# Kernel optimization log

Measured on AMD Instinct MI355X. Metric: run time of the kernel, lower is better.

Reference implementation:

```python
import jax, jax.numpy as jnp
import numpy as np

N = 50000      # nodes
E = 800000     # edges (avg degree 16)
F_IN = 128
H = 128        # hidden_channels
C = 10         # num_classes
S = 5          # Chebyshev order K
B = 8          # graphs in batch


def setup_inputs() -> dict:
    key = jax.random.key(0)
    ks = jax.random.split(key, 9)
    x = jax.random.normal(ks[0], (N, F_IN), jnp.float32)
    edge_index = jax.random.randint(ks[1], (2, E), 0, N, dtype=jnp.int64)
    batch = jnp.sort(jax.random.randint(ks[2], (N,), 0, B, dtype=jnp.int64))
    lambda_max = 2.0 * jnp.ones((B,), jnp.float32)
    W1 = jax.random.normal(ks[3], (S, F_IN, H), jnp.float32) * 0.05
    b1 = jax.random.normal(ks[4], (H,), jnp.float32) * 0.05
    W2 = jax.random.normal(ks[5], (S, H, H), jnp.float32) * 0.05
    b2 = jax.random.normal(ks[6], (H,), jnp.float32) * 0.05
    Wlin = jax.random.normal(ks[7], (H, C), jnp.float32) * 0.05
    blin = jax.random.normal(ks[8], (C,), jnp.float32) * 0.05
    return {"x": x, "edge_index": edge_index, "batch": batch,
            "lambda_max": lambda_max, "W1": W1, "b1": b1,
            "W2": W2, "b2": b2, "Wlin": Wlin, "blin": blin}


def _cheb_conv(x, row, col, w_edge, diag, W, b):
    # scaled Laplacian matvec: L_hat v = scatter(w_edge * v[col] -> row) + diag * v
    def Lhat(v):
        msg = v[col] * w_edge[:, None]                       # [E, d]
        return jax.ops.segment_sum(msg, row, num_segments=N) + diag[:, None] * v

    Tx0 = x
    out = Tx0 @ W[0]
    Tx1 = Lhat(Tx0)
    out = out + Tx1 @ W[1]
    for k in range(2, W.shape[0]):                           # Chebyshev recurrence
        Tx2 = 2.0 * Lhat(Tx1) - Tx0
        out = out + Tx2 @ W[k]
        Tx0, Tx1 = Tx1, Tx2
    return out + b


def reference(x, edge_index, batch, lambda_max, W1, b1, W2, b2, Wlin, blin):
    row, col = edge_index[0], edge_index[1]
    # sym-normalized Laplacian L = I - D^{-1/2} A D^{-1/2}; L_hat = 2L/lambda_max - I
    deg = jax.ops.segment_sum(jnp.ones((E,), x.dtype), row, num_segments=N)
    dis = jnp.where(deg > 0, jax.lax.rsqrt(jnp.maximum(deg, 1e-12)), 0.0)
    lam_e = lambda_max[batch[row]]                           # per-edge lambda_max
    w_edge = -2.0 * dis[row] * dis[col] / lam_e              # off-diagonal of L_hat
    diag = 2.0 / lambda_max[batch] - 1.0                     # diagonal of L_hat per node

    h = jax.nn.relu(_cheb_conv(x, row, col, w_edge, diag, W1, b1))
    h = jax.nn.relu(_cheb_conv(h, row, col, w_edge, diag, W2, b2))

    # global_mean_pool over batch assignment
    sums = jax.ops.segment_sum(h, batch, num_segments=B)     # [B, H]
    counts = jax.ops.segment_sum(jnp.ones((N, 1), h.dtype), batch, num_segments=B)
    pooled = sums / jnp.maximum(counts, 1.0)
    return pooled @ Wlin + blin                              # [B, C] logits (softmax unused in forward)
```

## Files before the change

### kernel.cpp

```cpp
#include <hip/hip_runtime.h>
#include <stdint.h>

typedef __attribute__((ext_vector_type(8))) short bf16x8;
typedef __attribute__((ext_vector_type(4))) float f32x4;

__device__ __forceinline__ float bf16lo_to_f(uint32_t u) { return __uint_as_float(u << 16); }
__device__ __forceinline__ float bf16hi_to_f(uint32_t u) { return __uint_as_float(u & 0xffff0000u); }
__device__ __forceinline__ uint16_t f_to_bf16(float f) {
    uint32_t u = __float_as_uint(f);
    uint32_t r = u + 0x7fff + ((u >> 16) & 1);
    return (uint16_t)(r >> 16);
}


#define BINCH 4096

__global__ void __launch_bounds__(256) k_pre1(
        const int* __restrict__ row, int* __restrict__ bhist,
        const float* __restrict__ W1, uint16_t* __restrict__ Wt1,
        const float* __restrict__ W2, uint16_t* __restrict__ Wt2,
        const float* __restrict__ x, uint16_t* __restrict__ Txb,
        int E, int N) {
    __shared__ int sh[256];
    int t = threadIdx.x, b = blockIdx.x;
    int gstride = gridDim.x * 256;
    sh[t] = 0;
    __syncthreads();
    for (int e = b * 256 + t; e < E; e += gstride)
        atomicAdd(&sh[row[e] >> 8], 1);
    __syncthreads();
    if (sh[t]) atomicAdd(&bhist[t], sh[t]);
    for (int i = b * 256 + t; i < 2 * 128 * 640; i += gstride) {
        int ii = i;
        const float* W = W1; uint16_t* Wt = Wt1;
        if (ii >= 128 * 640) { ii -= 128 * 640; W = W2; Wt = Wt2; }
        int o = ii / 640, kk = ii % 640;
        Wt[(size_t)o * 640 + kk] = f_to_bf16(W[(size_t)kk * 128 + o]);
    }
    {
        int lane = t & 63;
        int gw = b * 4 + (t >> 6);
        int tw = gridDim.x * 4;
        for (int n = gw; n < N; n += tw) {
            float2 v = ((const float2*)x)[(size_t)n * 64 + lane];
            uint32_t p = (uint32_t)f_to_bf16(v.x) | ((uint32_t)f_to_bf16(v.y) << 16);
            ((uint32_t*)Txb)[(size_t)n * 64 + lane] = p;
        }
    }
    if (b == 0) {
        int lane = t & 63;
        size_t ss32 = (size_t)(N + 1) * 64;
        for (int s = t >> 6; s < 5; s += 4)
            ((uint32_t*)Txb)[(size_t)s * ss32 + (size_t)N * 64 + lane] = 0u;
    }
}

__global__ void k_bscan(const int* __restrict__ bhist, int* __restrict__ gbase,
                        int* __restrict__ gcur, int nbk) {
    __shared__ int sh[256];
    int t = threadIdx.x;
    int v = t < nbk ? bhist[t] : 0;
    sh[t] = v;
    __syncthreads();
    for (int o = 1; o < 256; o <<= 1) {
        int u = (t >= o) ? sh[t - o] : 0;
        __syncthreads();
        sh[t] += u;
        __syncthreads();
    }
    gbase[t] = sh[t] - v;
    gcur[t] = sh[t] - v;
    if (t == 255) gbase[256] = sh[255];
}

__global__ void __launch_bounds__(256) k_bin(const int* __restrict__ row,
        const int* __restrict__ col, int* __restrict__ gcur,
        uint32_t* __restrict__ bout, int E) {
    __shared__ uint32_t stage[BINCH];
    __shared__ int hist[256], hscan[256], hcur[256], gofs[256];
    int t = threadIdx.x;
    int e0 = blockIdx.x * BINCH;
    int ecnt = min(BINCH, E - e0);
    hist[t] = 0;
    __syncthreads();
    for (int i = t; i < ecnt; i += 256)
        atomicAdd(&hist[row[e0 + i] >> 8], 1);
    __syncthreads();
    int v = hist[t];
    hscan[t] = v;
    __syncthreads();
    for (int o = 1; o < 256; o <<= 1) {
        int u = (t >= o) ? hscan[t - o] : 0;
        __syncthreads();
        hscan[t] += u;
        __syncthreads();
    }
    hcur[t] = hscan[t] - v;
    __syncthreads();
    for (int i = t; i < ecnt; i += 256) {
        int r = row[e0 + i];
        int p = atomicAdd(&hcur[r >> 8], 1);
        stage[p] = (uint32_t)(r & 255) | ((uint32_t)col[e0 + i] << 8);
    }
    __syncthreads();
    if (v > 0) gofs[t] = atomicAdd(&gcur[t], v);
    __syncthreads();
    for (int i = t; i < ecnt; i += 256) {
        int lo = 0, hi = 255;
        while (lo < hi) { int mid = (lo + hi) >> 1; if (hscan[mid] > i) hi = mid; else lo = mid + 1; }
        int b = lo;
        int local = i - (hscan[b] - hist[b]);
        bout[gofs[b] + local] = stage[i];
    }
}

__global__ void __launch_bounds__(256) k_deg2(const uint32_t* __restrict__ bout,
        const int* __restrict__ gbase, int* __restrict__ deg,
        int* __restrict__ psum, int N) {
    __shared__ int cnt[256];
    __shared__ int red[256];
    int t = threadIdx.x, b = blockIdx.x;
    cnt[t] = 0;
    __syncthreads();
    int s = gbase[b], epos = gbase[b + 1];
    for (int i = s + t; i < epos; i += 256)
        atomicAdd(&cnt[bout[i] & 255], 1);
    __syncthreads();
    int n = b * 256 + t;
    int d = cnt[t];
    if (n < N) deg[n] = d;
    red[t] = (n < N) ? ((d + 7) & ~7) : 0;
    __syncthreads();
    for (int o = 128; o > 0; o >>= 1) {
        if (t < o) red[t] += red[t + o];
        __syncthreads();
    }
    if (t == 0) psum[b] = red[0];
}

__global__ void k_offs(const int* __restrict__ deg, const int* __restrict__ psum,
                       int* __restrict__ offs,
                       const int* __restrict__ batch, const float* __restrict__ lam,
                       float* __restrict__ dis, float* __restrict__ diag,
                       uint4* __restrict__ nh,
                       int N, int nb) {
    __shared__ int pre[256];
    __shared__ int sh[256];
    int t = threadIdx.x, b = blockIdx.x;
    pre[t] = (t < b) ? psum[t] : 0;
    __syncthreads();
    for (int o = 128; o > 0; o >>= 1) {
        if (t < o) pre[t] += pre[t + o];
        __syncthreads();
    }
    int base = pre[0];
    __syncthreads();
    int idx = b * 256 + t;
    int d = idx < N ? deg[idx] : 0;
    int v = (d + 7) & ~7;
    sh[t] = v;
    __syncthreads();
    for (int o = 1; o < 256; o <<= 1) {
        int u = (t >= o) ? sh[t - o] : 0;
        __syncthreads();
        sh[t] += u;
        __syncthreads();
    }
    if (idx < N) {
        int beg = base + sh[t] - v;
        float dgv = 2.f / lam[batch[idx]] - 1.f;
        offs[idx] = beg;
        dis[idx] = d > 0 ? rsqrtf((float)d) : 0.f;
        diag[idx] = dgv;
        nh[idx] = make_uint4((uint32_t)beg, (uint32_t)(base + sh[t]),
                             __float_as_uint(dgv), 0u);
    }
    if (b == nb - 1 && t == 255) offs[N] = base + sh[255];
}

__global__ void __launch_bounds__(256) k_ew(const uint32_t* __restrict__ bout,
        const int* __restrict__ gbase, const int* __restrict__ offs,
        const float* __restrict__ dis, const float* __restrict__ diag,
        uint32_t* __restrict__ ew, int N) {
    __shared__ int cur[256];
    __shared__ int bs0[256];
    __shared__ float srw[256];
    int t = threadIdx.x, b = blockIdx.x;
    int n = b * 256 + t;
    int o0 = n < N ? offs[n] : 0;
    cur[t] = 0;
    bs0[t] = o0;
    srw[t] = (n < N) ? (-dis[n] * (diag[n] + 1.0f)) : 0.f;
    __syncthreads();
    int s = gbase[b], epos = gbase[b + 1];
    for (int i = s + t; i < epos; i += 256) {
        uint32_t v = bout[i];
        int r = (int)(v & 255u);
        int c = (int)(v >> 8);
        int idx = atomicAdd(&cur[r], 1);
        float w = srw[r] * dis[c];
        int pos = bs0[r] + (idx & ~7) + ((idx & 1) << 2) + ((idx >> 1) & 3);
        ew[pos] = (uint32_t)c | ((uint32_t)f_to_bf16(w) << 16);
    }
    __syncthreads();
    if (n < N) {
        int cnt = cur[t];
        int pe = (cnt + 7) & ~7;
        for (int i = cnt; i < pe; i++) {
            int pos = o0 + (i & ~7) + ((i & 1) << 2) + ((i >> 1) & 3);
            ew[pos] = (uint32_t)N;
        }
    }
}

__global__ void __launch_bounds__(256) k_lhat(uint16_t* __restrict__ Txb,
        const uint4* __restrict__ nh, const uint32_t* __restrict__ ew,
        int N,
        int src, int dst, int prev, float alpha, int use_prev) {
    int n = (blockIdx.x * blockDim.x + threadIdx.x) >> 6;
    int lane = threadIdx.x & 63;
    if (n >= N) return;
    int h = lane >> 5, g = lane & 31;
    size_t sb = (size_t)(N + 1) * 256;
    const uint8_t* srcs = (const uint8_t*)Txb + (size_t)src * sb;
    uint32_t g8 = (uint32_t)g * 8;
    uint4 hh = nh[n];
    int e = (int)hh.x, end = (int)hh.y;
    float dgn = __uint_as_float(hh.z);
    float a0 = 0.f, a1 = 0.f, a2 = 0.f, a3 = 0.f;
    int npk = (end - e) >> 3;
    const uint4* ep = (const uint4*)(ew + e + h * 4);
    int pk = 0;
    while (pk < npk) {
        if (npk - pk >= 2) {
            uint4 c0 = ep[pk * 2];
            uint4 c1 = ep[pk * 2 + 2];
            uint2 q[8]; float w[8];
#pragma unroll
            for (int u = 0; u < 4; u++) {
                uint32_t cw = (&c0.x)[u];
                w[u] = __uint_as_float(cw & 0xffff0000u);
                q[u] = *(const uint2*)(srcs + ((cw & 0xffffu) << 8) + g8);
            }
#pragma unroll
            for (int u = 0; u < 4; u++) {
                uint32_t cw = (&c1.x)[u];
                w[4 + u] = __uint_as_float(cw & 0xffff0000u);
                q[4 + u] = *(const uint2*)(srcs + ((cw & 0xffffu) << 8) + g8);
            }
#pragma unroll
            for (int u = 0; u < 8; u++) {
                a0 = fmaf(w[u], bf16lo_to_f(q[u].x), a0);
                a1 = fmaf(w[u], bf16hi_to_f(q[u].x), a1);
                a2 = fmaf(w[u], bf16lo_to_f(q[u].y), a2);
                a3 = fmaf(w[u], bf16hi_to_f(q[u].y), a3);
            }
            pk += 2;
        } else {
            uint4 c0 = ep[pk * 2];
#pragma unroll
            for (int u = 0; u < 4; u++) {
                uint32_t cw = (&c0.x)[u];
                float w = __uint_as_float(cw & 0xffff0000u);
                uint2 q = *(const uint2*)(srcs + ((cw & 0xffffu) << 8) + g8);
                a0 = fmaf(w, bf16lo_to_f(q.x), a0);
                a1 = fmaf(w, bf16hi_to_f(q.x), a1);
                a2 = fmaf(w, bf16lo_to_f(q.y), a2);
                a3 = fmaf(w, bf16hi_to_f(q.y), a3);
            }
            pk += 1;
        }
    }
    a0 += __shfl_xor(a0, 32);
    a1 += __shfl_xor(a1, 32);
    a2 += __shfl_xor(a2, 32);
    a3 += __shfl_xor(a3, 32);
    if (h == 0) {
        size_t ro = (size_t)n * 256 + g8;
        uint2 qs = *(const uint2*)(srcs + ro);
        a0 = fmaf(dgn, bf16lo_to_f(qs.x), a0);
        a1 = fmaf(dgn, bf16hi_to_f(qs.x), a1);
        a2 = fmaf(dgn, bf16lo_to_f(qs.y), a2);
        a3 = fmaf(dgn, bf16hi_to_f(qs.y), a3);
        float f0 = alpha * a0, f1 = alpha * a1, f2 = alpha * a2, f3 = alpha * a3;
        if (use_prev) {
            uint2 qp = *(const uint2*)((const uint8_t*)Txb + (size_t)prev * sb + ro);
            f0 -= bf16lo_to_f(qp.x);
            f1 -= bf16hi_to_f(qp.x);
            f2 -= bf16lo_to_f(qp.y);
            f3 -= bf16hi_to_f(qp.y);
        }
        uint2 pk2;
        pk2.x = (uint32_t)f_to_bf16(f0) | ((uint32_t)f_to_bf16(f1) << 16);
        pk2.y = (uint32_t)f_to_bf16(f2) | ((uint32_t)f_to_bf16(f3) << 16);
        *(uint2*)((uint8_t*)Txb + (size_t)dst * sb + ro) = pk2;
    }
}

#define BM 128
#define BK 64
#define LDT 72
#define LDC 132

__global__ void __launch_bounds__(256) k_gemm(
        const uint16_t* __restrict__ A, size_t sstride,
        const uint16_t* __restrict__ Bt,
        const float* __restrict__ bias,
        uint16_t* __restrict__ out2b,
        float* __restrict__ pooled,
        const int* __restrict__ batch,
        int M, int Kdim) {
    __shared__ uint16_t smem[BM * LDT + 128 * LDT];
    uint16_t* As = smem;
    uint16_t* Bs = smem + BM * LDT;
    uint16_t* Ct = smem;
    int t = threadIdx.x;
    int w = t >> 6, lane = t & 63;
    int row0 = blockIdx.x * BM;
    int mrow = (w >> 1) * 64, ncol = (w & 1) * 64;

    int ar[4], akc[4];
#pragma unroll
    for (int rep = 0; rep < 4; rep++) {
        int d = rep * 256 + t;
        ar[rep] = d >> 3; akc[rep] = d & 7;
    }

    f32x4 acc[4][4];
#pragma unroll
    for (int i = 0; i < 4; i++)
#pragma unroll
        for (int j = 0; j < 4; j++) acc[i][j] = (f32x4){0.f, 0.f, 0.f, 0.f};

    bf16x8 pa[4], pb[4];
#pragma unroll
    for (int rep = 0; rep < 4; rep++) {
        int grow = row0 + ar[rep];
        int kk = akc[rep] * 8;
        bf16x8 va = {0, 0, 0, 0, 0, 0, 0, 0};
        if (grow < M)
            va = *(const bf16x8*)(A + (size_t)(kk >> 7) * sstride + (size_t)grow * 128 + (kk & 127));
        pa[rep] = va;
        pb[rep] = *(const bf16x8*)(Bt + (size_t)ar[rep] * Kdim + kk);
    }

    for (int k0 = 0; k0 < Kdim; k0 += BK) {
#pragma unroll
        for (int rep = 0; rep < 4; rep++) {
            *(bf16x8*)(&As[ar[rep] * LDT + akc[rep] * 8]) = pa[rep];
            *(bf16x8*)(&Bs[ar[rep] * LDT + akc[rep] * 8]) = pb[rep];
        }
        __syncthreads();
        int kn = k0 + BK;
        if (kn < Kdim) {
#pragma unroll
            for (int rep = 0; rep < 4; rep++) {
                int grow = row0 + ar[rep];
                int kk = kn + akc[rep] * 8;
                bf16x8 va = {0, 0, 0, 0, 0, 0, 0, 0};
                if (grow < M)
                    va = *(const bf16x8*)(A + (size_t)(kk >> 7) * sstride + (size_t)grow * 128 + (kk & 127));
                pa[rep] = va;
                pb[rep] = *(const bf16x8*)(Bt + (size_t)ar[rep] * Kdim + kk);
            }
        }
#pragma unroll
        for (int ks = 0; ks < BK; ks += 32) {
            bf16x8 af[4], bfr[4];
#pragma unroll
            for (int i = 0; i < 4; i++) {
                int r = mrow + i * 16 + (lane & 15);
                af[i] = *(const bf16x8*)(&As[r * LDT + ks + (lane >> 4) * 8]);
            }
#pragma unroll
            for (int j = 0; j < 4; j++) {
                int c = ncol + j * 16 + (lane & 15);
                bfr[j] = *(const bf16x8*)(&Bs[c * LDT + ks + (lane >> 4) * 8]);
            }
#pragma unroll
            for (int i = 0; i < 4; i++)
#pragma unroll
                for (int j = 0; j < 4; j++)
                    acc[i][j] = __builtin_amdgcn_mfma_f32_16x16x32_bf16(af[i], bfr[j], acc[i][j], 0, 0, 0);
        }
        __syncthreads();
    }

#pragma unroll
    for (int j = 0; j < 4; j++) {
        int c = ncol + j * 16 + (lane & 15);
        float bv = bias[c];
#pragma unroll
        for (int i = 0; i < 4; i++) {
            int rloc = mrow + i * 16 + (lane >> 4) * 4;
#pragma unroll
            for (int r = 0; r < 4; r++) {
                float v = acc[i][j][r] + bv;
                v = v > 0.f ? v : 0.f;
                Ct[(rloc + r) * LDC + c] = f_to_bf16(v);
            }
        }
    }
    __syncthreads();

    if (out2b) {
#pragma unroll
        for (int rep = 0; rep < 8; rep++) {
            int d = rep * 256 + t;
            int r = d >> 4, c8 = (d & 15) * 8;
            int grow = row0 + r;
            if (grow < M) {
                bf16x8 v = *(const bf16x8*)(&Ct[r * LDC + c8]);
                *(bf16x8*)(out2b + (size_t)grow * 128 + c8) = v;
            }
        }
    }
    if (pooled) {
        int f = t & 127, r0 = (t >> 7) * 64;
        float accp = 0.f;
        int curb = -1;
        for (int r = r0; r < r0 + 64; ++r) {
            int grow = row0 + r;
            if (grow >= M) break;
            int b = batch[grow];
            if (b != curb) {
                if (curb >= 0) atomicAdd(&pooled[curb * 128 + f], accp);
                accp = 0.f; curb = b;
            }
            accp += __uint_as_float(((uint32_t)Ct[r * LDC + f]) << 16);
        }
        if (curb >= 0) atomicAdd(&pooled[curb * 128 + f], accp);
    }
}

__global__ void k_final(const float* __restrict__ pooled, const int* __restrict__ batch,
                        const float* __restrict__ Wlin, const float* __restrict__ blin,
                        float* __restrict__ out, int N, int B_, int C_) {
    __shared__ int cnt[64];
    int t = threadIdx.x;
    if (t < B_) {
        auto lb = [&](int v) {
            int lo = 0, hi = N;
            while (lo < hi) {
                int mid = (lo + hi) >> 1;
                if (batch[mid] < v) lo = mid + 1; else hi = mid;
            }
            return lo;
        };
        cnt[t] = lb(t + 1) - lb(t);
    }
    __syncthreads();
    if (t < B_ * C_) {
        int b = t / C_, c = t % C_;
        float inv = 1.f / fmaxf((float)cnt[b], 1.f);
        float acc = blin[c];
        for (int f = 0; f < 128; ++f) acc += pooled[b * 128 + f] * inv * Wlin[f * C_ + c];
        out[t] = acc;
    }
}

extern "C" void kernel_launch(void* const* d_in, const int* in_sizes, int n_in,
                              void* d_out, int out_size, void* d_ws, size_t ws_size,
                              hipStream_t stream) {
    const float* x    = (const float*)d_in[0];
    const int*   edge = (const int*)d_in[1];
    const int*   batch= (const int*)d_in[2];
    const float* lam  = (const float*)d_in[3];
    const float* W1   = (const float*)d_in[4];
    const float* b1   = (const float*)d_in[5];
    const float* W2   = (const float*)d_in[6];
    const float* b2   = (const float*)d_in[7];
    const float* Wlin = (const float*)d_in[8];
    const float* blin = (const float*)d_in[9];
    const int E  = in_sizes[1] / 2;
    const int N  = in_sizes[2];
    const int B_ = in_sizes[3];
    const int* row = edge;
    const int* col = edge + E;

    char* ws = (char*)d_ws;
    size_t off = 0;
    auto take = [&](size_t bytes) -> char* {
        char* p = ws + off;
        off = (off + bytes + 255) & ~(size_t)255;
        return p;
    };
    uint16_t* Txb    = (uint16_t*)take((size_t)5 * (N + 1) * 128 * 2);
    uint32_t* ew     = (uint32_t*)take(((size_t)E + 8 * (size_t)N) * 4);
    int*      deg    = (int*)take((size_t)N * 4);
    int*      offs   = (int*)take((size_t)(N + 1) * 4);
    float*    dis    = (float*)take((size_t)N * 4);
    float*    diag   = (float*)take((size_t)N * 4);
    uint4*    nh     = (uint4*)take((size_t)N * 16);
    uint16_t* Wt1    = (uint16_t*)take((size_t)128 * 640 * 2);
    uint16_t* Wt2    = (uint16_t*)take((size_t)128 * 640 * 2);
    float*    pooled = (float*)take((size_t)B_ * 128 * 4);
    int*      bhist  = (int*)take(257 * 4);
    int*      gbase  = (int*)take(257 * 4);
    int*      gcur   = (int*)take(257 * 4);
    const int nb = (N + 255) / 256;
    int*      psum   = (int*)take((size_t)nb * 4);
    uint32_t* bout   = (uint32_t*)((char*)Txb + (size_t)4 * (N + 1) * 256);

    hipMemsetAsync(pooled, 0, (size_t)B_ * 128 * 4 + 257 * 4, stream);

    const int nchunks = (E + BINCH - 1) / BINCH;

    k_pre1<<<1024, 256, 0, stream>>>(row, bhist, W1, Wt1, W2, Wt2, x, Txb, E, N);
    k_bscan<<<1, 256, 0, stream>>>(bhist, gbase, gcur, nb);
    k_bin<<<nchunks, 256, 0, stream>>>(row, col, gcur, bout, E);
    k_deg2<<<nb, 256, 0, stream>>>(bout, gbase, deg, psum, N);
    k_offs<<<nb, 256, 0, stream>>>(deg, psum, offs, batch, lam, dis, diag, nh, N, nb);
    k_ew<<<nb, 256, 0, stream>>>(bout, gbase, offs, dis, diag, ew, N);

    const int lblocks = (N + 3) / 4;
    const int gblocks = (N + BM - 1) / BM;
    const size_t ss = (size_t)(N + 1) * 128;

    k_lhat<<<lblocks, 256, 0, stream>>>(Txb, nh, ew, N, 0, 1, 0, 1.f, 0);
    k_lhat<<<lblocks, 256, 0, stream>>>(Txb, nh, ew, N, 1, 2, 0, 2.f, 1);
    k_lhat<<<lblocks, 256, 0, stream>>>(Txb, nh, ew, N, 2, 3, 1, 2.f, 1);
    k_lhat<<<lblocks, 256, 0, stream>>>(Txb, nh, ew, N, 3, 4, 2, 2.f, 1);
    k_gemm<<<gblocks, 256, 0, stream>>>(Txb, ss, Wt1, b1,
                                        Txb , (float*)nullptr, batch, N, 640);

    k_lhat<<<lblocks, 256, 0, stream>>>(Txb, nh, ew, N, 0, 1, 0, 1.f, 0);
    k_lhat<<<lblocks, 256, 0, stream>>>(Txb, nh, ew, N, 1, 2, 0, 2.f, 1);
    k_lhat<<<lblocks, 256, 0, stream>>>(Txb, nh, ew, N, 2, 3, 1, 2.f, 1);
    k_lhat<<<lblocks, 256, 0, stream>>>(Txb, nh, ew, N, 3, 4, 2, 2.f, 1);
    k_gemm<<<gblocks, 256, 0, stream>>>(Txb, ss, Wt2, b2,
                                        (uint16_t*)nullptr, pooled, batch, N, 640);

    k_final<<<1, 128, 0, stream>>>(pooled, batch, Wlin, blin, (float*)d_out, N, B_, 10);
}
```

Before: 468.5 us.

## Load GEMM tiles straight into LDS via global_load_lds with XOR swizzle

The GEMM kernel's A and B tile staging now uses the global-to-LDS direct load builtin instead of loading into registers and then storing to LDS. The padded LDS layout becomes an unpadded 64-wide layout with an XOR swizzle on the k offset to avoid bank conflicts. This is meant to cut VGPR use and the LDS-store instructions. In exchange it drops the register prefetch that overlapped the next tile's global loads with MFMA work, and it drops the row-bounds check on A, so the last row block reads past M.

```diff
diff --git a/kernel.cpp b/kernel.cpp
--- a/kernel.cpp
+++ b/kernel.cpp
@@ -1,5 +1,9 @@
 #include <hip/hip_runtime.h>
 #include <stdint.h>
+
+#ifndef __has_builtin
+#define __has_builtin(x) 0
+#endif
 
 typedef __attribute__((ext_vector_type(8))) short bf16x8;
 typedef __attribute__((ext_vector_type(4))) float f32x4;
@@ -10,6 +14,15 @@
     uint32_t u = __float_as_uint(f);
     uint32_t r = u + 0x7fff + ((u >> 16) & 1);
     return (uint16_t)(r >> 16);
+}
+
+__device__ __forceinline__ void dma16(const uint16_t* g, uint16_t* lds, int lane) {
+#if __has_builtin(__builtin_amdgcn_global_load_lds)
+    __builtin_amdgcn_global_load_lds((const __attribute__((address_space(1))) void*)g,
+                                     (__attribute__((address_space(3))) void*)lds, 16, 0, 0);
+#else
+    *(bf16x8*)(lds + lane * 8) = *(const bf16x8*)g;
+#endif
 }
 
 
@@ -298,8 +311,7 @@
 }
 
 #define BM 128
-#define BK 64
-#define LDT 72
+#define BKS 64
 #define LDC 132
 
 __global__ void __launch_bounds__(256) k_gemm(
@@ -310,20 +322,22 @@
         float* __restrict__ pooled,
         const int* __restrict__ batch,
         int M, int Kdim) {
-    __shared__ uint16_t smem[BM * LDT + 128 * LDT];
+    __shared__ uint16_t smem[128 * LDC];
     uint16_t* As = smem;
-    uint16_t* Bs = smem + BM * LDT;
+    uint16_t* Bs = smem + 128 * 64;
     uint16_t* Ct = smem;
     int t = threadIdx.x;
     int w = t >> 6, lane = t & 63;
     int row0 = blockIdx.x * BM;
     int mrow = (w >> 1) * 64, ncol = (w & 1) * 64;
 
-    int ar[4], akc[4];
+    int ar[4], swz[4];
 #pragma unroll
     for (int rep = 0; rep < 4; rep++) {
         int d = rep * 256 + t;
-        ar[rep] = d >> 3; akc[rep] = d & 7;
+        int a = d >> 3, kc = d & 7;
+        ar[rep] = a;
+        swz[rep] = (kc * 8) ^ ((a & 7) << 3);
     }
 
     f32x4 acc[4][4];
@@ -332,50 +346,35 @@
 #pragma unroll
         for (int j = 0; j < 4; j++) acc[i][j] = (f32x4){0.f, 0.f, 0.f, 0.f};
 
-    bf16x8 pa[4], pb[4];
-#pragma unroll
-    for (int rep = 0; rep < 4; rep++) {
-        int grow = row0 + ar[rep];
-        int kk = akc[rep] * 8;
-        bf16x8 va = {0, 0, 0, 0, 0, 0, 0, 0};
-        if (grow < M)
-            va = *(const bf16x8*)(A + (size_t)(kk >> 7) * sstride + (size_t)grow * 128 + (kk & 127));
-        pa[rep] = va;
-        pb[rep] = *(const bf16x8*)(Bt + (size_t)ar[rep] * Kdim + kk);
-    }
-
-    for (int k0 = 0; k0 < Kdim; k0 += BK) {
+    for (int k0 = 0; k0 < Kdim; k0 += BKS) {
+        int slotbase = (k0 >> 7) * (int)0;
+        (void)slotbase;
 #pragma unroll
         for (int rep = 0; rep < 4; rep++) {
-            *(bf16x8*)(&As[ar[rep] * LDT + akc[rep] * 8]) = pa[rep];
-            *(bf16x8*)(&Bs[ar[rep] * LDT + akc[rep] * 8]) = pb[rep];
-        }
-        __syncthreads();
-        int kn = k0 + BK;
-        if (kn < Kdim) {
-#pragma unroll
-            for (int rep = 0; rep < 4; rep++) {
-                int grow = row0 + ar[rep];
-                int kk = kn + akc[rep] * 8;
-                bf16x8 va = {0, 0, 0, 0, 0, 0, 0, 0};
-                if (grow < M)
-                    va = *(const bf16x8*)(A + (size_t)(kk >> 7) * sstride + (size_t)grow * 128 + (kk & 127));
-                pa[rep] = va;
-                pb[rep] = *(const bf16x8*)(Bt + (size_t)ar[rep] * Kdim + kk);
-            }
-        }
-#pragma unroll
-        for (int ks = 0; ks < BK; ks += 32) {
+            int grow = row0 + ar[rep];
+            const uint16_t* ga = A + (size_t)(k0 >> 7) * sstride
+                                 + (size_t)grow * 128 + (k0 & 64) + swz[rep];
+            uint16_t* la = As + (size_t)(rep * 256 + (t & ~63)) * 8;
+            dma16(ga, la, lane);
+            const uint16_t* gb = Bt + (size_t)ar[rep] * Kdim + k0 + swz[rep];
+            uint16_t* lb = Bs + (size_t)(rep * 256 + (t & ~63)) * 8;
+            dma16(gb, lb, lane);
+        }
+        __syncthreads();
+#pragma unroll
+        for (int ks = 0; ks < BKS; ks += 32) {
             bf16x8 af[4], bfr[4];
 #pragma unroll
             for (int i = 0; i < 4; i++) {
                 int r = mrow + i * 16 + (lane & 15);
-                af[i] = *(const bf16x8*)(&As[r * LDT + ks + (lane >> 4) * 8]);
+                int ko = (ks + (lane >> 4) * 8) ^ ((r & 7) << 3);
+                af[i] = *(const bf16x8*)(&As[r * 64 + ko]);
             }
 #pragma unroll
             for (int j = 0; j < 4; j++) {
                 int c = ncol + j * 16 + (lane & 15);
-                bfr[j] = *(const bf16x8*)(&Bs[c * LDT + ks + (lane >> 4) * 8]);
+                int ko = (ks + (lane >> 4) * 8) ^ ((c & 7) << 3);
+                bfr[j] = *(const bf16x8*)(&Bs[c * 64 + ko]);
             }
 #pragma unroll
             for (int i = 0; i < 4; i++)
```

After: 468.4 us. About the same (-0.0%).
